# Kernel optimization log

Measured on AMD Instinct MI355X. Metric: run time of the kernel, lower is better.

## Reference

```python
import jax, jax.numpy as jnp
import numpy as np

KS = 64      # kernel_size
NFFT = 64    # n_fft
IC = 32      # in_channel
OC = 64      # out_channel
B, T1, T2 = 4, 4096, 512


def setup_inputs() -> dict:
    key = jax.random.key(0)
    k1, k2, k3, k4 = jax.random.split(key, 4)
    x = jax.random.normal(k1, (B, T1, IC), dtype=jnp.float32)
    # continuous index in [0, T1-1)
    index = jax.random.uniform(k2, (B, T2), dtype=jnp.float32) * (T1 - 1)
    kb = 1.0 / np.sqrt(KS * IC)  # matches reset_parameters uniform bound
    kernel = jax.random.uniform(k3, (OC, IC, NFFT), minval=-kb, maxval=kb, dtype=jnp.float32)
    bias = jax.random.uniform(k4, (OC,), minval=-kb, maxval=kb, dtype=jnp.float32)
    return {"x": x, "index": index, "kernel": kernel, "bias": bias}


def reference(x, index, kernel, bias):
    # fractional-delay kernel per (b, t2) via FFT phase shift
    i = jnp.floor(index).astype(jnp.int32)          # (b, t2) integer part
    f = index - jnp.floor(index)                    # (b, t2) fractional part
    freqs = jnp.arange(NFFT // 2 + 1)               # rfft bins
    shift = jnp.exp(2j * jnp.pi * f[..., None] * freqs / NFFT)   # (b, t2, nf)
    K = jnp.fft.rfft(kernel)                        # (oc, ic, nf)
    K = K[None, None] * shift[:, :, None, None, :]  # (b, t2, oc, ic, nf)
    ker = jnp.fft.irfft(K, n=KS)                    # (b, t2, oc, ic, ks)

    # gather centered length-ks windows of x at integer positions i
    pad = KS // 2
    x_pad = jnp.pad(x, ((0, 0), (pad, pad), (0, 0)))            # (b, t1+2p, ic)
    pos = i[:, :, None] + jnp.arange(KS)[None, None, :]          # (b, t2, ks)
    barr = jnp.arange(x.shape[0])[:, None, None]
    xwin = x_pad[barr, pos]                                      # (b, t2, ks, ic)

    # per-position matmul: out[b,t,o] = sum_{c,k} ker[b,t,o,c,k] * xwin[b,t,k,c]
    out = jnp.einsum('btock,btkc->bto', ker, xwin) + bias
    return out
```

## Files before the change

kernel.cpp:

```cpp
#include <hip/hip_runtime.h>
#include <hip/hip_bf16.h>
#include <math.h>

#define B_   4
#define T1_  4096
#define T2_  512
#define IC_  32
#define OC_  64
#define KS_  64

typedef unsigned short u16;
typedef unsigned int   u32;
typedef __attribute__((ext_vector_type(8))) short  short8;
typedef __attribute__((ext_vector_type(4))) float  float4v;

__device__ __forceinline__ u16 f2bf(float f) {
    union { u32 u; float f; } v; v.f = f;
    u32 u = v.u;
    return (u16)((u + 0x7FFFu + ((u >> 16) & 1u)) >> 16);
}

#define PI_F 3.14159265358979323846f

__global__ __launch_bounds__(256) void prep_interp_kernel(
        const float* __restrict__ x, const float* __restrict__ index,
        const float* __restrict__ kern, u16* __restrict__ Y,
        u16* __restrict__ Bsz)
{
    __shared__ __align__(16) float xwT[2][IC_][68];
    __shared__ __align__(16) float wsh[2][64];

    const int tid = threadIdx.x;

    if (blockIdx.x < 64) {
        int gid = blockIdx.x * 256 + tid;
        int o   = gid & 63;
        int cs8 = gid >> 6;
        const float* p = kern + (size_t)o * 2048 + cs8 * 8;
        float4 a = *(const float4*)p;
        float4 b = *(const float4*)(p + 4);
        u16* q = Bsz + (size_t)cs8 * 512 + o * 8;
        *(ushort4*)(q)     = make_ushort4(f2bf(a.x), f2bf(a.y), f2bf(a.z), f2bf(a.w));
        *(ushort4*)(q + 4) = make_ushort4(f2bf(b.x), f2bf(b.y), f2bf(b.z), f2bf(b.w));
        return;
    }

    const int p2 = blockIdx.x - 64;

    #pragma unroll
    for (int h = 0; h < 2; ++h) {
        const int bt = p2 * 2 + h;
        const int b  = bt >> 9;
        float fidx = index[bt];
        float flo  = floorf(fidx);
        int   i0   = (int)flo;
        float f    = fidx - flo;

        int e  = tid * 8;
        int k  = e >> 5;
        int c0 = e & 31;
        int pos = i0 + k - 32;
        float vals[8];
        if (pos >= 0 && pos < T1_) {
            const float* p = x + ((size_t)(b * T1_ + pos) * IC_ + c0);
            float4 a = *(const float4*)p;
            float4 d = *(const float4*)(p + 4);
            vals[0]=a.x; vals[1]=a.y; vals[2]=a.z; vals[3]=a.w;
            vals[4]=d.x; vals[5]=d.y; vals[6]=d.z; vals[7]=d.w;
        } else {
            #pragma unroll
            for (int q = 0; q < 8; ++q) vals[q] = 0.0f;
        }
        #pragma unroll
        for (int q = 0; q < 8; ++q) xwT[h][c0 + q][k] = vals[q];

        if (tid < 64) {
            int j = tid;
            float wj;
            if (f <= 0.0f) {
                wj = (j == 0) ? 1.0f : 0.0f;
            } else {
                float spf = sinf(PI_F * f);
                float a   = PI_F * ((float)j + f) * (1.0f / 64.0f);
                wj = ((j & 1) ? -spf : spf) * cosf(a) / (64.0f * sinf(a));
            }
            wsh[h][j] = wj;
        }
    }
    __syncthreads();

    const int h   = tid >> 7;
    const int rem = tid & 127;
    const int c   = rem >> 2;
    const int s0  = (rem & 3) << 4;

    float xr[64];
    #pragma unroll
    for (int q = 0; q < 16; ++q) {
        int idx = (s0 + q * 4) & 63;
        const float4 v = *(const float4*)&xwT[h][c][idx];
        xr[q*4+0] = v.x; xr[q*4+1] = v.y; xr[q*4+2] = v.z; xr[q*4+3] = v.w;
    }

    float acc[16];
    #pragma unroll
    for (int r = 0; r < 16; ++r) acc[r] = 0.0f;

    #pragma unroll
    for (int jq = 0; jq < 16; ++jq) {
        const float4 wv = *(const float4*)&wsh[h][jq * 4];
        #pragma unroll
        for (int jj = 0; jj < 4; ++jj) {
            const float wj = (jj == 0) ? wv.x : (jj == 1) ? wv.y : (jj == 2) ? wv.z : wv.w;
            const int j = jq * 4 + jj;
            #pragma unroll
            for (int r = 0; r < 16; ++r)
                acc[r] += wj * xr[(j + r) & 63];
        }
    }

    const int bt = p2 * 2 + h;
    union { u16 u[8]; short8 v; } o0, o1;
    #pragma unroll
    for (int r = 0; r < 8; ++r) { o0.u[r] = f2bf(acc[r]); o1.u[r] = f2bf(acc[8 + r]); }
    u16* yp = Y + ((size_t)bt * 2048 + c * 64 + s0);
    *(short8*)(yp)     = o0.v;
    *(short8*)(yp + 8) = o1.v;
}

__global__ __launch_bounds__(512, 2) void gemm_kernel(const u16* __restrict__ Y,
                                                      const u16* __restrict__ Bsz,
                                                      const float* __restrict__ bias,
                                                      float* __restrict__ out)
{
    __shared__ float red[8][4][8][17];

    const int tid  = threadIdx.x;
    const int w    = tid >> 6;
    const int lane = tid & 63;
    const int nm   = lane & 15;
    const int q    = lane >> 4;
    const int g    = blockIdx.x;

    const int rr  = nm & 7;
    const int p2  = (g & 7) + 8 * (4 * (g >> 3) + (rr >> 1));
    const int btA = 2 * p2 + (rr & 1);

    const int kb0 = w * 8;
    const u16* aptr = Y   + (size_t)btA * 2048 + kb0 * 32 + q * 8;
    const u16* bptr = Bsz + (size_t)kb0 * 2048 + q * 512 + nm * 8;

    short8 a[8], b[8][4];
    #pragma unroll
    for (int i = 0; i < 8; ++i) {
        a[i] = *(const short8*)(aptr + i * 32);
        #pragma unroll
        for (int n = 0; n < 4; ++n)
            b[i][n] = *(const short8*)(bptr + (size_t)i * 2048 + n * 128);
    }
    if (nm >= 8) {
        const short8 zz = {0,0,0,0,0,0,0,0};
        #pragma unroll
        for (int i = 0; i < 8; ++i) a[i] = zz;
    }

    float4v acc0 = {0,0,0,0}, acc1 = {0,0,0,0}, acc2 = {0,0,0,0}, acc3 = {0,0,0,0};
    #pragma unroll
    for (int i = 0; i < 8; ++i) {
        acc0 = __builtin_amdgcn_mfma_f32_16x16x32_bf16(a[i], b[i][0], acc0, 0, 0, 0);
        acc1 = __builtin_amdgcn_mfma_f32_16x16x32_bf16(a[i], b[i][1], acc1, 0, 0, 0);
        acc2 = __builtin_amdgcn_mfma_f32_16x16x32_bf16(a[i], b[i][2], acc2, 0, 0, 0);
        acc3 = __builtin_amdgcn_mfma_f32_16x16x32_bf16(a[i], b[i][3], acc3, 0, 0, 0);
    }

    if (q < 2) {
        #pragma unroll
        for (int r = 0; r < 4; ++r) {
            const int row = q * 4 + r;
            red[w][0][row][nm] = acc0[r];
            red[w][1][row][nm] = acc1[r];
            red[w][2][row][nm] = acc2[r];
            red[w][3][row][nm] = acc3[r];
        }
    }
    __syncthreads();

    {
        const int row = tid >> 6;
        const int o   = tid & 63;
        float s = bias[o];
        #pragma unroll
        for (int ww = 0; ww < 8; ++ww)
            s += red[ww][o >> 4][row][o & 15];
        const int p2o = (g & 7) + 8 * (4 * (g >> 3) + (row >> 1));
        const int bto = 2 * p2o + (row & 1);
        out[(size_t)bto * 64 + o] = s;
    }
}

extern "C" void kernel_launch(void* const* d_in, const int* in_sizes, int n_in,
                              void* d_out, int out_size, void* d_ws, size_t ws_size,
                              hipStream_t stream)
{
    const float* x     = (const float*)d_in[0];
    const float* index = (const float*)d_in[1];
    const float* kern  = (const float*)d_in[2];
    const float* bias  = (const float*)d_in[3];
    float* out = (float*)d_out;

    u16* Y   = (u16*)d_ws;
    u16* Bsz = (u16*)((char*)d_ws + (size_t)8 * 1024 * 1024);

    prep_interp_kernel<<<dim3(64 + B_ * T2_ / 2), dim3(256), 0, stream>>>(x, index, kern, Y, Bsz);
    gemm_kernel<<<dim3(256), dim3(512), 0, stream>>>(Y, Bsz, bias, out);
}
```

Before: 75.49 us.

## Compute circular interpolation convolution with MFMA, one position per wavefront

The prep kernel's circular convolution of each 64-tap x window with the sinc-like weights moves from scalar FP32 FMAs into bf16 MFMA instructions. A circulant weight matrix is built from a padded weight vector in shared memory, and the x window is gathered straight from global memory into B fragments. Each wavefront now handles one (b,t2) position, so a block covers four positions, and the gemm kernel's row-to-position mapping is updated to match. This removes the large per-thread register FMA loop and the LDS transpose, but quantises the weights and x to bf16 before the convolution instead of after, and the gathers are scalar, uncoalesced global loads.

```diff
diff --git a/kernel.cpp b/kernel.cpp
--- a/kernel.cpp
+++ b/kernel.cpp
@@ -27,8 +27,7 @@
         const float* __restrict__ kern, u16* __restrict__ Y,
         u16* __restrict__ Bsz)
 {
-    __shared__ __align__(16) float xwT[2][IC_][68];
-    __shared__ __align__(16) float wsh[2][64];
+    __shared__ __align__(16) float w2[4][76];
 
     const int tid = threadIdx.x;
 
@@ -45,87 +44,91 @@
         return;
     }
 
-    const int p2 = blockIdx.x - 64;
-
-    #pragma unroll
-    for (int h = 0; h < 2; ++h) {
-        const int bt = p2 * 2 + h;
-        const int b  = bt >> 9;
-        float fidx = index[bt];
-        float flo  = floorf(fidx);
-        int   i0   = (int)flo;
-        float f    = fidx - flo;
-
-        int e  = tid * 8;
-        int k  = e >> 5;
-        int c0 = e & 31;
-        int pos = i0 + k - 32;
-        float vals[8];
-        if (pos >= 0 && pos < T1_) {
-            const float* p = x + ((size_t)(b * T1_ + pos) * IC_ + c0);
-            float4 a = *(const float4*)p;
-            float4 d = *(const float4*)(p + 4);
-            vals[0]=a.x; vals[1]=a.y; vals[2]=a.z; vals[3]=a.w;
-            vals[4]=d.x; vals[5]=d.y; vals[6]=d.z; vals[7]=d.w;
+    const int pb   = blockIdx.x - 64;
+    const int wv   = tid >> 6;
+    const int lane = tid & 63;
+    const int bt   = pb * 4 + wv;
+    const int b    = bt >> 9;
+
+    const float fidx = index[bt];
+    const float flo  = floorf(fidx);
+    const int   i0   = (int)flo;
+    const float f    = fidx - flo;
+
+    {
+        const int t = lane;
+        float wj;
+        if (f <= 0.0f) {
+            wj = (t == 0) ? 1.0f : 0.0f;
         } else {
+            float spf = sinf(PI_F * f);
+            float a   = PI_F * ((float)t + f) * (1.0f / 64.0f);
+            wj = ((t & 1) ? -spf : spf) * cosf(a) / (64.0f * sinf(a));
+        }
+        w2[wv][t] = wj;
+        if (t < 8) w2[wv][64 + t] = wj;
+    }
+
+    const int nm = lane & 15;
+    const int q  = lane >> 4;
+
+    short8 Afr[4];
+    #pragma unroll
+    for (int d = 0; d < 4; ++d) {
+        const int o0 = (16 * d + q * 8 - nm) & 63;
+        const float* wp = &w2[wv][o0];
+        union { u16 u[8]; short8 s; } cv;
+        #pragma unroll
+        for (int j = 0; j < 8; ++j) cv.u[j] = f2bf(wp[j]);
+        Afr[d] = cv.s;
+    }
+
+    short8 Bfr[2][2];
+    #pragma unroll
+    for (int kb = 0; kb < 2; ++kb) {
+        #pragma unroll
+        for (int nt = 0; nt < 2; ++nt) {
+            const int c = nt * 16 + nm;
+            union { u16 u[8]; short8 s; } cv;
             #pragma unroll
-            for (int q = 0; q < 8; ++q) vals[q] = 0.0f;
-        }
-        #pragma unroll
-        for (int q = 0; q < 8; ++q) xwT[h][c0 + q][k] = vals[q];
-
-        if (tid < 64) {
-            int j = tid;
-            float wj;
-            if (f <= 0.0f) {
-                wj = (j == 0) ? 1.0f : 0.0f;
-            } else {
-                float spf = sinf(PI_F * f);
-                float a   = PI_F * ((float)j + f) * (1.0f / 64.0f);
-                wj = ((j & 1) ? -spf : spf) * cosf(a) / (64.0f * sinf(a));
+            for (int j = 0; j < 8; ++j) {
+                int pos = i0 - 32 + kb * 32 + q * 8 + j;
+                int pc  = min(max(pos, 0), T1_ - 1);
+                float v = x[(size_t)(b * T1_ + pc) * IC_ + c];
+                v = ((unsigned)pos < (unsigned)T1_) ? v : 0.0f;
+                cv.u[j] = f2bf(v);
             }
-            wsh[h][j] = wj;
-        }
-    }
-    __syncthreads();
-
-    const int h   = tid >> 7;
-    const int rem = tid & 127;
-    const int c   = rem >> 2;
-    const int s0  = (rem & 3) << 4;
-
-    float xr[64];
-    #pragma unroll
-    for (int q = 0; q < 16; ++q) {
-        int idx = (s0 + q * 4) & 63;
-        const float4 v = *(const float4*)&xwT[h][c][idx];
-        xr[q*4+0] = v.x; xr[q*4+1] = v.y; xr[q*4+2] = v.z; xr[q*4+3] = v.w;
-    }
-
-    float acc[16];
-    #pragma unroll
-    for (int r = 0; r < 16; ++r) acc[r] = 0.0f;
-
-    #pragma unroll
-    for (int jq = 0; jq < 16; ++jq) {
-        const float4 wv = *(const float4*)&wsh[h][jq * 4];
-        #pragma unroll
-        for (int jj = 0; jj < 4; ++jj) {
-            const float wj = (jj == 0) ? wv.x : (jj == 1) ? wv.y : (jj == 2) ? wv.z : wv.w;
-            const int j = jq * 4 + jj;
+            Bfr[kb][nt] = cv.s;
+        }
+    }
+
+    float4v acc[4][2];
+    #pragma unroll
+    for (int mt = 0; mt < 4; ++mt)
+        #pragma unroll
+        for (int nt = 0; nt < 2; ++nt)
+            acc[mt][nt] = (float4v){0.f, 0.f, 0.f, 0.f};
+    #pragma unroll
+    for (int kb = 0; kb < 2; ++kb)
+        #pragma unroll
+        for (int mt = 0; mt < 4; ++mt) {
+            const int d = (2 * kb - mt) & 3;
             #pragma unroll
-            for (int r = 0; r < 16; ++r)
-                acc[r] += wj * xr[(j + r) & 63];
-        }
-    }
-
-    const int bt = p2 * 2 + h;
-    union { u16 u[8]; short8 v; } o0, o1;
-    #pragma unroll
-    for (int r = 0; r < 8; ++r) { o0.u[r] = f2bf(acc[r]); o1.u[r] = f2bf(acc[8 + r]); }
-    u16* yp = Y + ((size_t)bt * 2048 + c * 64 + s0);
-    *(short8*)(yp)     = o0.v;
-    *(short8*)(yp + 8) = o1.v;
+            for (int nt = 0; nt < 2; ++nt)
+                acc[mt][nt] = __builtin_amdgcn_mfma_f32_16x16x32_bf16(
+                                  Afr[d], Bfr[kb][nt], acc[mt][nt], 0, 0, 0);
+        }
+
+    #pragma unroll
+    for (int mt = 0; mt < 4; ++mt)
+        #pragma unroll
+        for (int nt = 0; nt < 2; ++nt) {
+            const int c = nt * 16 + nm;
+            const int s = mt * 16 + q * 4;
+            u32 d0 = (u32)f2bf(acc[mt][nt][0]) | ((u32)f2bf(acc[mt][nt][1]) << 16);
+            u32 d1 = (u32)f2bf(acc[mt][nt][2]) | ((u32)f2bf(acc[mt][nt][3]) << 16);
+            *(uint2*)(Y + (size_t)bt * 2048 + c * 64 + s) = make_uint2(d0, d1);
+        }
 }
 
 __global__ __launch_bounds__(512, 2) void gemm_kernel(const u16* __restrict__ Y,
@@ -143,8 +146,8 @@
     const int g    = blockIdx.x;
 
     const int rr  = nm & 7;
-    const int p2  = (g & 7) + 8 * (4 * (g >> 3) + (rr >> 1));
-    const int btA = 2 * p2 + (rr & 1);
+    const int pbA = (g & 7) + 8 * (2 * (g >> 3) + (rr >> 2));
+    const int btA = 4 * pbA + (rr & 3);
 
     const int kb0 = w * 8;
     const u16* aptr = Y   + (size_t)btA * 2048 + kb0 * 32 + q * 8;
@@ -192,8 +195,8 @@
         #pragma unroll
         for (int ww = 0; ww < 8; ++ww)
             s += red[ww][o >> 4][row][o & 15];
-        const int p2o = (g & 7) + 8 * (4 * (g >> 3) + (row >> 1));
-        const int bto = 2 * p2o + (row & 1);
+        const int pbo = (g & 7) + 8 * (2 * (g >> 3) + (row >> 2));
+        const int bto = 4 * pbo + (row & 3);
         out[(size_t)bto * 64 + o] = s;
     }
 }
@@ -211,6 +214,6 @@
     u16* Y   = (u16*)d_ws;
     u16* Bsz = (u16*)((char*)d_ws + (size_t)8 * 1024 * 1024);
 
-    prep_interp_kernel<<<dim3(64 + B_ * T2_ / 2), dim3(256), 0, stream>>>(x, index, kern, Y, Bsz);
+    prep_interp_kernel<<<dim3(64 + B_ * T2_ / 4), dim3(256), 0, stream>>>(x, index, kern, Y, Bsz);
     gemm_kernel<<<dim3(256), dim3(512), 0, stream>>>(Y, Bsz, bias, out);
 }
```

After: 72.17 us. 1.05x faster.
